# Optimization experiments

Hardware: AMD Instinct MI355X
Metric: run time of the kernel (lower is better)

## Reference

```python
import jax, jax.numpy as jnp
import numpy as np

EMBED_DIM = 1024
NUM_HEADS = 16
HEAD_DIM = EMBED_DIM // NUM_HEADS
RANK = 512
B, S = 4, 4096


def setup_inputs() -> dict:
    key = jax.random.key(0)
    ks = jax.random.split(key, 16)
    sd = 0.02
    inp = {
        "query": jax.random.normal(ks[0], (B, S, EMBED_DIM), jnp.float32),
        "key": jax.random.normal(ks[1], (B, S, EMBED_DIM), jnp.float32),
        "value": jax.random.normal(ks[2], (B, S, EMBED_DIM), jnp.float32),
        # torch nn.Linear weights: [out_features, in_features]
        "q_down_w": jax.random.normal(ks[3], (RANK, EMBED_DIM), jnp.float32) * sd,
        "q_up_w": jax.random.normal(ks[4], (EMBED_DIM, RANK), jnp.float32) * sd,
        "q_up_b": jax.random.normal(ks[5], (EMBED_DIM,), jnp.float32) * sd,
        "k_down_w": jax.random.normal(ks[6], (RANK, EMBED_DIM), jnp.float32) * sd,
        "k_up_w": jax.random.normal(ks[7], (EMBED_DIM, RANK), jnp.float32) * sd,
        "k_up_b": jax.random.normal(ks[8], (EMBED_DIM,), jnp.float32) * sd,
        "v_down_w": jax.random.normal(ks[9], (RANK, EMBED_DIM), jnp.float32) * sd,
        "v_up_w": jax.random.normal(ks[10], (EMBED_DIM, RANK), jnp.float32) * sd,
        "v_up_b": jax.random.normal(ks[11], (EMBED_DIM,), jnp.float32) * sd,
        "out_w": jax.random.normal(ks[12], (EMBED_DIM, EMBED_DIM), jnp.float32) * sd,
        "out_b": jax.random.normal(ks[13], (EMBED_DIM,), jnp.float32) * sd,
    }
    return inp


def _linear(x, w, b=None):
    y = x @ w.T
    return y if b is None else y + b


def reference(query, key, value,
              q_down_w, q_up_w, q_up_b,
              k_down_w, k_up_w, k_up_b,
              v_down_w, v_up_w, v_up_b,
              out_w, out_b):
    b, s, _ = query.shape
    # low-rank QKV projections
    q = _linear(_linear(query, q_down_w), q_up_w, q_up_b)
    k = _linear(_linear(key, k_down_w), k_up_w, k_up_b)
    v = _linear(_linear(value, v_down_w), v_up_w, v_up_b)
    # [B,S,E] -> [B,H,S,Dh]
    q = q.reshape(b, s, NUM_HEADS, HEAD_DIM).transpose(0, 2, 1, 3)
    k = k.reshape(b, s, NUM_HEADS, HEAD_DIM).transpose(0, 2, 1, 3)
    v = v.reshape(b, s, NUM_HEADS, HEAD_DIM).transpose(0, 2, 1, 3)
    # kernel feature map: elu + 1  (note: scaling_factor in original is computed but unused)
    q = jax.nn.elu(q) + 1.0
    k = jax.nn.elu(k) + 1.0
    k_sum = k.sum(axis=-2)                              # [B,H,Dh]
    denom = jnp.einsum('bhnd,bhd->bhn', q, k_sum)       # [B,H,S]
    kv = jnp.einsum('bhnd,bhne->bhde', k, v)            # [B,H,Dh,Dh]
    num = jnp.einsum('bhnd,bhde->bhne', q, kv)          # [B,H,S,Dh]
    out = num / (denom[..., None] + 1e-6)
    out = out.transpose(0, 2, 1, 3).reshape(b, s, EMBED_DIM)
    return _linear(out, out_w, out_b)
```

## Files before the change

### kernel.cpp

```cpp
#include <hip/hip_runtime.h>
#include <hip/hip_bf16.h>

typedef unsigned short ushort_t;
typedef unsigned int uint_t;
typedef __attribute__((ext_vector_type(8))) short short8;
typedef __attribute__((ext_vector_type(4))) float f32x4;
typedef __attribute__((ext_vector_type(2))) float f32x2;

#define EMBED 1024
#define RANK  512
#define BB    4
#define SS    4096
#define HH    16
#define DHD   64
#define MM    (BB*SS)
#define NCHUNK 16

__device__ __forceinline__ float bf2f(ushort_t u) {
    union { uint_t i; float f; } v; v.i = ((uint_t)u) << 16; return v.f;
}
__device__ __forceinline__ float asf(uint_t u) {
    union { uint_t i; float f; } v; v.i = u; return v.f;
}
__device__ __forceinline__ ushort_t f2bf(float f) {
    union { float f; uint_t i; } v; v.f = f;
    uint_t r = v.i + 0x7FFFu + ((v.i >> 16) & 1u);
    return (ushort_t)(r >> 16);
}
__device__ __forceinline__ uint_t cvtpk(float lo, float hi) {
    uint_t r;
    asm("v_cvt_pk_bf16_f32 %0, %1, %2" : "=v"(r) : "v"(lo), "v"(hi));
    return r;
}
__device__ __forceinline__ void gl2lds16(const void* g, void* l) {
    __builtin_amdgcn_global_load_lds((const __attribute__((address_space(1))) void*)g,
                                     (__attribute__((address_space(3))) void*)l,
                                     16, 0, 0);
}

template<int EPI>
__global__ __launch_bounds__(256) void gemm_bt(
    const ushort_t* __restrict__ A0, const ushort_t* __restrict__ A1, const ushort_t* __restrict__ A2,
    const ushort_t* __restrict__ B0, const ushort_t* __restrict__ B1, const ushort_t* __restrict__ B2,
    const float* __restrict__ bias0, const float* __restrict__ bias1, const float* __restrict__ bias2,
    void* __restrict__ C0, void* __restrict__ C1, void* __restrict__ C2,
    int N, int K, int nbx)
{
    __shared__ __align__(16) char lds_raw[49152];

    const int z = blockIdx.z;
    const ushort_t* Ab   = (z == 0) ? A0 : (z == 1) ? A1 : A2;
    const ushort_t* Bm   = (z == 0) ? B0 : (z == 1) ? B1 : B2;
    const float*    bias = (z == 0) ? bias0 : (z == 1) ? bias1 : bias2;
    void*           Cv   = (z == 0) ? C0 : (z == 1) ? C1 : C2;

    const int cpx = gridDim.x >> 3;
    const int bid = blockIdx.x;
    const int wg  = (bid & 7) * cpx + (bid >> 3);
    const long m0 = (long)(wg / nbx) * 128;
    const long n0 = (long)(wg % nbx) * 128;

    const int t = threadIdx.x;
    const int lane = t & 63;
    const int w = t >> 6;
    const int wr = (w >> 1) * 64;
    const int wc = (w & 1) * 64;
    const int fr = lane & 15;
    const int kq = (lane >> 4) * 8;

    const int srow = t >> 2;
    const int scol = ((t & 3) ^ ((srow >> 1) & 3)) * 8;
    const int kqs = (((kq >> 3) ^ ((fr >> 1) & 3))) * 8;

    auto STAGE = [&](int k0, int buf) {
        char* Ad = lds_raw + buf * 8192;
        char* Bd = lds_raw + 24576 + buf * 8192;
        #pragma unroll
        for (int ro = 0; ro < 2; ++ro) {
            const int row = ro * 64 + srow;
            gl2lds16(Ab + (m0 + row) * (long)K + k0 + scol, Ad + (ro * 256 + w * 64) * 16);
            gl2lds16(Bm + (n0 + row) * (long)K + k0 + scol, Bd + (ro * 256 + w * 64) * 16);
        }
    };

    f32x4 acc[4][4] = {};
    const int nt = K >> 5;

    STAGE(0, 0);
    STAGE(32, 1);

    int cur = 0;
    for (int ti = 0; ti < nt; ++ti) {
        if (ti + 1 < nt) { asm volatile("s_waitcnt vmcnt(4)" ::: "memory"); }
        else             { asm volatile("s_waitcnt vmcnt(0)" ::: "memory"); }
        __builtin_amdgcn_sched_barrier(0);
        __builtin_amdgcn_s_barrier();
        __builtin_amdgcn_sched_barrier(0);

        int nb = cur + 2; if (nb >= 3) nb -= 3;
        if (ti + 2 < nt) STAGE((ti + 2) << 5, nb);

        const ushort_t* Asc = (const ushort_t*)(lds_raw + cur * 8192);
        const ushort_t* Bsc = (const ushort_t*)(lds_raw + 24576 + cur * 8192);
        short8 av[4], bv[4];
        #pragma unroll
        for (int mi = 0; mi < 4; ++mi)
            av[mi] = *(const short8*)&Asc[(wr + mi * 16 + fr) * 32 + kqs];
        #pragma unroll
        for (int nf = 0; nf < 4; ++nf)
            bv[nf] = *(const short8*)&Bsc[(wc + nf * 16 + fr) * 32 + kqs];
        #pragma unroll
        for (int mi = 0; mi < 4; ++mi)
            #pragma unroll
            for (int nf = 0; nf < 4; ++nf)
                acc[mi][nf] = __builtin_amdgcn_mfma_f32_16x16x32_bf16(
                    av[mi], bv[nf], acc[mi][nf], 0, 0, 0);

        ++cur; if (cur == 3) cur = 0;
    }

    const int rj = (lane >> 4) * 4;
    if (EPI == 3) {
        float* Cf = (float*)Cv;
        __syncthreads();
        #pragma unroll
        for (int nf = 0; nf < 4; ++nf) {
            const long col = n0 + wc + nf * 16 + fr;
            const float bval = bias[col];
            #pragma unroll
            for (int mi = 0; mi < 4; ++mi)
                #pragma unroll
                for (int j = 0; j < 4; ++j)
                    Cf[(m0 + wr + mi * 16 + rj + j) * (long)N + col] = acc[mi][nf][j] + bval;
        }
    } else {
        ushort_t* Ct = (ushort_t*)lds_raw;
        __syncthreads();
        const bool do_elu = (EPI == 2) && (z < 2);
        #pragma unroll
        for (int nf = 0; nf < 4; ++nf) {
            const int coll = wc + nf * 16 + fr;
            const float bval = (EPI >= 2) ? bias[n0 + coll] : 0.0f;
            #pragma unroll
            for (int mi = 0; mi < 4; ++mi) {
                #pragma unroll
                for (int j = 0; j < 4; ++j) {
                    float x = acc[mi][nf][j];
                    if (EPI >= 2) x += bval;
                    if (do_elu) x = (x > 0.0f) ? (x + 1.0f) : __expf(x);
                    Ct[(wr + mi * 16 + rj + j) * 136 + coll] = f2bf(x);
                }
            }
        }
        __syncthreads();
        ushort_t* Cb = (ushort_t*)Cv;
        #pragma unroll
        for (int it = 0; it < 8; ++it) {
            const int idx = it * 256 + t;
            const int r   = idx >> 4;
            const int c8  = (idx & 15) * 8;
            short8 vv = *(const short8*)&Ct[r * 136 + c8];
            *(short8*)(Cb + (m0 + r) * (long)N + n0 + c8) = vv;
        }
    }
}

__global__ __launch_bounds__(256) void gemm_dn(
    const float* __restrict__ A0, const float* __restrict__ A1, const float* __restrict__ A2,
    const ushort_t* __restrict__ B0, const ushort_t* __restrict__ B1, const ushort_t* __restrict__ B2,
    void* __restrict__ C0, void* __restrict__ C1, void* __restrict__ C2,
    int N, int K, int nbx)
{
    __shared__ __align__(16) char lds_raw[73728];

    const int z = blockIdx.z;
    const float*    Af = (z == 0) ? A0 : (z == 1) ? A1 : A2;
    const ushort_t* Bm = (z == 0) ? B0 : (z == 1) ? B1 : B2;
    void*           Cv = (z == 0) ? C0 : (z == 1) ? C1 : C2;

    const int cpx = gridDim.x >> 3;
    const int bid = blockIdx.x;
    const int wg  = (bid & 7) * cpx + (bid >> 3);
    const long m0 = (long)(wg / nbx) * 128;
    const long n0 = (long)(wg % nbx) * 128;

    const int t = threadIdx.x;
    const int lane = t & 63;
    const int w = t >> 6;
    const int wr = (w >> 1) * 64;
    const int wc = (w & 1) * 64;
    const int fr = lane & 15;
    const int kq4 = lane >> 4;
    const int fx  = fr & 7;

    const int srow = t >> 2;
    const int scol = ((t & 3) ^ ((srow >> 1) & 3)) * 8;
    const int kqs = ((kq4 ^ ((fr >> 1) & 3))) * 8;

    const int sArow = t >> 3;
    const int sAcol = ((t & 7) ^ (sArow & 7)) * 4;

    auto STAGE = [&](int k0, int buf) {
        char* Ad = lds_raw + buf * 16384;
        char* Bd = lds_raw + 49152 + buf * 8192;
        #pragma unroll
        for (int p = 0; p < 4; ++p)
            gl2lds16(Af + (m0 + p * 32 + sArow) * (long)K + k0 + sAcol,
                     Ad + p * 4096 + w * 1024);
        #pragma unroll
        for (int ro = 0; ro < 2; ++ro)
            gl2lds16(Bm + (n0 + ro * 64 + srow) * (long)K + k0 + scol,
                     Bd + (ro * 256 + w * 64) * 16);
    };

    f32x4 acc[4][4] = {};
    const int nt = K >> 5;

    STAGE(0, 0);
    STAGE(32, 1);

    int cur = 0;
    for (int ti = 0; ti < nt; ++ti) {
        if (ti + 1 < nt) { asm volatile("s_waitcnt vmcnt(6)" ::: "memory"); }
        else             { asm volatile("s_waitcnt vmcnt(0)" ::: "memory"); }
        __builtin_amdgcn_sched_barrier(0);
        __builtin_amdgcn_s_barrier();
        __builtin_amdgcn_sched_barrier(0);

        int nb = cur + 2; if (nb >= 3) nb -= 3;
        if (ti + 2 < nt) STAGE((ti + 2) << 5, nb);

        const float*    Asf = (const float*)(lds_raw + cur * 16384);
        const ushort_t* Bsc = (const ushort_t*)(lds_raw + 49152 + cur * 8192);

        short8 av[4], bv[4];
        #pragma unroll
        for (int mi = 0; mi < 4; ++mi) {
            const int rowoff = (wr + mi * 16 + fr) * 32;
            const int s0 = (2 * kq4) ^ fx;
            const int s1 = (2 * kq4 + 1) ^ fx;
            f32x4 a0 = *(const f32x4*)&Asf[rowoff + s0 * 4];
            f32x4 a1 = *(const f32x4*)&Asf[rowoff + s1 * 4];
            union { uint_t u[4]; short8 s; } pk;
            pk.u[0] = cvtpk(a0[0], a0[1]);
            pk.u[1] = cvtpk(a0[2], a0[3]);
            pk.u[2] = cvtpk(a1[0], a1[1]);
            pk.u[3] = cvtpk(a1[2], a1[3]);
            av[mi] = pk.s;
        }
        #pragma unroll
        for (int nf = 0; nf < 4; ++nf)
            bv[nf] = *(const short8*)&Bsc[(wc + nf * 16 + fr) * 32 + kqs];
        #pragma unroll
        for (int mi = 0; mi < 4; ++mi)
            #pragma unroll
            for (int nf = 0; nf < 4; ++nf)
                acc[mi][nf] = __builtin_amdgcn_mfma_f32_16x16x32_bf16(
                    av[mi], bv[nf], acc[mi][nf], 0, 0, 0);

        ++cur; if (cur == 3) cur = 0;
    }

    const int rj = kq4 * 4;
    ushort_t* Ct = (ushort_t*)lds_raw;
    __syncthreads();
    #pragma unroll
    for (int nf = 0; nf < 4; ++nf) {
        const int coll = wc + nf * 16 + fr;
        #pragma unroll
        for (int mi = 0; mi < 4; ++mi)
            #pragma unroll
            for (int j = 0; j < 4; ++j)
                Ct[(wr + mi * 16 + rj + j) * 136 + coll] = f2bf(acc[mi][nf][j]);
    }
    __syncthreads();
    ushort_t* Cb = (ushort_t*)Cv;
    #pragma unroll
    for (int it = 0; it < 8; ++it) {
        const int idx = it * 256 + t;
        const int r   = idx >> 4;
        const int c8  = (idx & 15) * 8;
        short8 vv = *(const short8*)&Ct[r * 136 + c8];
        *(short8*)(Cb + (m0 + r) * (long)N + n0 + c8) = vv;
    }
}

__global__ __launch_bounds__(256) void cvt_weights(
    const float* __restrict__ s0, const float* __restrict__ s1,
    const float* __restrict__ s2, const float* __restrict__ s3,
    const float* __restrict__ s4, const float* __restrict__ s5,
    const float* __restrict__ s6,
    ushort_t* __restrict__ d0, ushort_t* __restrict__ d1,
    ushort_t* __restrict__ d2, ushort_t* __restrict__ d3,
    ushort_t* __restrict__ d4, ushort_t* __restrict__ d5,
    ushort_t* __restrict__ d6)
{
    const int y = blockIdx.y;
    const float* src; ushort_t* dst; int n;
    switch (y) {
        case 0: src = s0; dst = d0; n = RANK * EMBED; break;
        case 1: src = s1; dst = d1; n = RANK * EMBED; break;
        case 2: src = s2; dst = d2; n = RANK * EMBED; break;
        case 3: src = s3; dst = d3; n = RANK * EMBED; break;
        case 4: src = s4; dst = d4; n = RANK * EMBED; break;
        case 5: src = s5; dst = d5; n = RANK * EMBED; break;
        default: src = s6; dst = d6; n = EMBED * EMBED; break;
    }
    const int i = (blockIdx.x * 256 + threadIdx.x) * 4;
    if (i < n) {
        f32x4 f = *(const f32x4*)(src + i);
        typedef __attribute__((ext_vector_type(4))) short short4v;
        short4v h;
        h[0] = (short)f2bf(f[0]); h[1] = (short)f2bf(f[1]);
        h[2] = (short)f2bf(f[2]); h[3] = (short)f2bf(f[3]);
        *(short4v*)(dst + i) = h;
    }
}

__global__ __launch_bounds__(256) void kv_stats(const ushort_t* __restrict__ Kp,
                                                const ushort_t* __restrict__ Vp,
                                                float* __restrict__ kvp,
                                                float* __restrict__ ksump)
{
    __shared__ __align__(16) ushort_t Ks[64 * 64];
    __shared__ __align__(16) ushort_t Vs[64 * 64];
    const int t = threadIdx.x;
    const int w = t >> 6;
    const int bh = blockIdx.x;
    const int chunk = blockIdx.y;
    const int b = bh >> 4, h = bh & 15;
    const int d0 = (t & 15) * 4;
    const int e0 = (t >> 4) * 4;
    f32x2 acc2[4][2] = {};
    f32x2 sks2[2] = {};
    const long hbase = ((long)b * SS) * EMBED + h * DHD;

    for (int sub = 0; sub < 4; ++sub) {
        const int n00 = chunk * 256 + sub * 64;
        #pragma unroll
        for (int ro = 0; ro < 2; ++ro) {
            const int idx = ro * 256 + t;
            const int r = idx >> 3, c16 = idx & 7;
            const long g = hbase + (long)(n00 + r) * EMBED + c16 * 8;
            gl2lds16(Kp + g, (char*)Ks + (ro * 256 + w * 64) * 16);
            gl2lds16(Vp + g, (char*)Vs + (ro * 256 + w * 64) * 16);
        }
        __syncthreads();
        #pragma unroll 8
        for (int n = 0; n < 64; ++n) {
            const uint_t* kr = (const uint_t*)(Ks + n * 64 + d0);
            const uint_t* vr = (const uint_t*)(Vs + n * 64 + e0);
            const uint_t k01 = kr[0], k23 = kr[1];
            const uint_t v01 = vr[0], v23 = vr[1];
            f32x2 kd0, kd1;
            kd0[0] = asf(k01 << 16); kd0[1] = asf(k01 & 0xffff0000u);
            kd1[0] = asf(k23 << 16); kd1[1] = asf(k23 & 0xffff0000u);
            float ve[4];
            ve[0] = asf(v01 << 16); ve[1] = asf(v01 & 0xffff0000u);
            ve[2] = asf(v23 << 16); ve[3] = asf(v23 & 0xffff0000u);
            #pragma unroll
            for (int e = 0; e < 4; ++e) {
                f32x2 vb; vb[0] = ve[e]; vb[1] = ve[e];
                acc2[e][0] += vb * kd0;
                acc2[e][1] += vb * kd1;
            }
            if (e0 == 0) { sks2[0] += kd0; sks2[1] += kd1; }
        }
        __syncthreads();
    }

    float* dst = kvp + ((long)chunk * 64 + bh) * 4096;
    #pragma unroll
    for (int e = 0; e < 4; ++e) {
        f32x4 vv;
        vv[0] = acc2[e][0][0]; vv[1] = acc2[e][0][1];
        vv[2] = acc2[e][1][0]; vv[3] = acc2[e][1][1];
        *(f32x4*)(dst + (e0 + e) * 64 + d0) = vv;
    }
    if (e0 == 0) {
        float* sd = ksump + ((long)chunk * 64 + bh) * 64 + d0;
        sd[0] = sks2[0][0]; sd[1] = sks2[0][1];
        sd[2] = sks2[1][0]; sd[3] = sks2[1][1];
    }
}

__global__ __launch_bounds__(256) void kv_reduce(const float* __restrict__ kvp,
                                                 const float* __restrict__ ksump,
                                                 ushort_t* __restrict__ kvb,
                                                 float* __restrict__ ksumf)
{
    const int bh = blockIdx.x;
    const int t = threadIdx.x;
    const long base = (long)bh * 4096 + t * 16;
    f32x4 s[4] = {};
    #pragma unroll 4
    for (int c = 0; c < NCHUNK; ++c) {
        const float* src = kvp + (long)c * 64 * 4096 + base;
        #pragma unroll
        for (int j = 0; j < 4; ++j) s[j] += *(const f32x4*)(src + j * 4);
    }
    short8 o0, o1;
    #pragma unroll
    for (int j = 0; j < 4; ++j) {
        o0[j]     = (short)f2bf(s[0][j]); o0[4 + j] = (short)f2bf(s[1][j]);
        o1[j]     = (short)f2bf(s[2][j]); o1[4 + j] = (short)f2bf(s[3][j]);
    }
    *(short8*)(kvb + base)     = o0;
    *(short8*)(kvb + base + 8) = o1;

    if (t < 64) {
        float ss = 0.f;
        #pragma unroll
        for (int c = 0; c < NCHUNK; ++c) ss += ksump[(long)c * 64 * 64 + bh * 64 + t];
        ksumf[bh * 64 + t] = ss;
    }
}

__global__ __launch_bounds__(256) void attn_out(const ushort_t* __restrict__ Qp,
                                                const ushort_t* __restrict__ kvb,
                                                const float* __restrict__ ksum,
                                                ushort_t* __restrict__ Op)
{
    __shared__ __align__(16) ushort_t Qs[128 * 64];
    __shared__ __align__(16) ushort_t KVs[64 * 64];
    __shared__ float kss[64];
    __shared__ float dnm[128];
    const int t = threadIdx.x;
    const int w = t >> 6, lane = t & 63;
    const int bh = blockIdx.x, mc = blockIdx.y;
    const int b = bh >> 4, h = bh & 15;
    const long base = ((long)b * SS + mc * 128) * EMBED + h * DHD;

    #pragma unroll
    for (int ro = 0; ro < 4; ++ro) {
        const int idx = ro * 256 + t;
        const int r = idx >> 3, c16 = idx & 7;
        gl2lds16(Qp + base + (long)r * EMBED + c16 * 8,
                 (char*)Qs + (ro * 256 + w * 64) * 16);
    }
    #pragma unroll
    for (int ro = 0; ro < 2; ++ro) {
        const int idx = ro * 256 + t;
        gl2lds16(kvb + (long)bh * 4096 + idx * 8,
                 (char*)KVs + (ro * 256 + w * 64) * 16);
    }
    if (t < 64) kss[t] = ksum[bh * 64 + t];
    __syncthreads();

    if (t < 128) {
        float s = 0.f;
        const uint_t* qr = (const uint_t*)(Qs + t * 64);
        #pragma unroll
        for (int jj = 0; jj < 32; ++jj) {
            const uint_t u = qr[jj];
            union { uint_t i; float f; } lo, hi;
            lo.i = u << 16; hi.i = u & 0xffff0000u;
            s += lo.f * kss[2 * jj] + hi.f * kss[2 * jj + 1];
        }
        dnm[t] = s;
    }

    const int fr = lane & 15, kq = (lane >> 4) * 8;
    f32x4 acc[2][4] = {};
    #pragma unroll
    for (int ks = 0; ks < 2; ++ks) {
        short8 av[2], bv[4];
        #pragma unroll
        for (int mi = 0; mi < 2; ++mi)
            av[mi] = *(const short8*)&Qs[(w * 32 + mi * 16 + fr) * 64 + ks * 32 + kq];
        #pragma unroll
        for (int nf = 0; nf < 4; ++nf)
            bv[nf] = *(const short8*)&KVs[(nf * 16 + fr) * 64 + ks * 32 + kq];
        #pragma unroll
        for (int mi = 0; mi < 2; ++mi)
            #pragma unroll
            for (int nf = 0; nf < 4; ++nf)
                acc[mi][nf] = __builtin_amdgcn_mfma_f32_16x16x32_bf16(
                    av[mi], bv[nf], acc[mi][nf], 0, 0, 0);
    }
    __syncthreads();

    const int rj = (lane >> 4) * 4;
    #pragma unroll
    for (int mi = 0; mi < 2; ++mi) {
        #pragma unroll
        for (int nf = 0; nf < 4; ++nf) {
            #pragma unroll
            for (int j = 0; j < 4; ++j) {
                const int r = w * 32 + mi * 16 + rj + j;
                const int c = nf * 16 + fr;
                const float x = acc[mi][nf][j] / (dnm[r] + 1e-6f);
                Op[base + (long)r * EMBED + c] = f2bf(x);
            }
        }
    }
}

extern "C" void kernel_launch(void* const* d_in, const int* in_sizes, int n_in,
                              void* d_out, int out_size, void* d_ws, size_t ws_size,
                              hipStream_t stream)
{
    (void)in_sizes; (void)n_in; (void)out_size; (void)ws_size;
    const float* query = (const float*)d_in[0];
    const float* key_  = (const float*)d_in[1];
    const float* value = (const float*)d_in[2];
    const float* q_dw  = (const float*)d_in[3];
    const float* q_uw  = (const float*)d_in[4];
    const float* q_ub  = (const float*)d_in[5];
    const float* k_dw  = (const float*)d_in[6];
    const float* k_uw  = (const float*)d_in[7];
    const float* k_ub  = (const float*)d_in[8];
    const float* v_dw  = (const float*)d_in[9];
    const float* v_uw  = (const float*)d_in[10];
    const float* v_ub  = (const float*)d_in[11];
    const float* o_w   = (const float*)d_in[12];
    const float* o_b   = (const float*)d_in[13];

    char* ws = (char*)d_ws;
    size_t off = 0;
    auto alloc = [&](size_t bytes) -> void* {
        void* p = ws + off;
        off += (bytes + 255) & ~(size_t)255;
        return p;
    };
    const size_t WSMALL = (size_t)RANK * EMBED;
    ushort_t* bw_qd = (ushort_t*)alloc(WSMALL * 2);
    ushort_t* bw_qu = (ushort_t*)alloc(WSMALL * 2);
    ushort_t* bw_kd = (ushort_t*)alloc(WSMALL * 2);
    ushort_t* bw_ku = (ushort_t*)alloc(WSMALL * 2);
    ushort_t* bw_vd = (ushort_t*)alloc(WSMALL * 2);
    ushort_t* bw_vu = (ushort_t*)alloc(WSMALL * 2);
    ushort_t* bw_o  = (ushort_t*)alloc((size_t)EMBED * EMBED * 2);
    ushort_t* PQ    = (ushort_t*)alloc((size_t)MM * EMBED * 2);
    ushort_t* PK    = (ushort_t*)alloc((size_t)MM * EMBED * 2);
    ushort_t* PV    = (ushort_t*)alloc((size_t)MM * EMBED * 2);
    ushort_t* Y1q   = (ushort_t*)alloc((size_t)MM * RANK * 2);
    ushort_t* Y1k   = (ushort_t*)alloc((size_t)MM * RANK * 2);
    ushort_t* Y1v   = (ushort_t*)alloc((size_t)MM * RANK * 2);
    float*    ksump = (float*)alloc((size_t)NCHUNK * 64 * 64 * 4);
    float*    ksumf = (float*)alloc((size_t)64 * 64 * 4);
    ushort_t* kvb   = (ushort_t*)alloc((size_t)64 * 64 * 64 * 2);

    float*    kvp = (float*)Y1q;
    ushort_t* O   = Y1k;

    const dim3 blk(256);

    cvt_weights<<<dim3(EMBED * EMBED / 1024, 7), blk, 0, stream>>>(
        q_dw, q_uw, k_dw, k_uw, v_dw, v_uw, o_w,
        bw_qd, bw_qu, bw_kd, bw_ku, bw_vd, bw_vu, bw_o);

    gemm_dn<<<dim3(MM / 128 * (RANK / 128), 1, 3), blk, 0, stream>>>(
        query, key_, value,
        bw_qd, bw_kd, bw_vd,
        Y1q, Y1k, Y1v,
        RANK, EMBED, RANK / 128);

    gemm_bt<2><<<dim3(MM / 128 * (EMBED / 128), 1, 3), blk, 0, stream>>>(
        Y1q, Y1k, Y1v,
        bw_qu, bw_ku, bw_vu,
        q_ub, k_ub, v_ub,
        PQ, PK, PV,
        EMBED, RANK, EMBED / 128);

    kv_stats<<<dim3(64, NCHUNK), blk, 0, stream>>>(PK, PV, kvp, ksump);
    kv_reduce<<<dim3(64), blk, 0, stream>>>(kvp, ksump, kvb, ksumf);
    attn_out<<<dim3(64, 32), blk, 0, stream>>>(PQ, kvb, ksumf, O);

    gemm_bt<3><<<dim3(MM / 128 * (EMBED / 128), 1, 1), blk, 0, stream>>>(
        O, nullptr, nullptr,
        bw_o, nullptr, nullptr,
        o_b, nullptr, nullptr,
        d_out, nullptr, nullptr,
        EMBED, EMBED, EMBED / 128);
}
```

Measured before the change: 302.3 us.

## Convert fp32 A tiles to bf16 in registers before LDS staging in gemm_dn

The down-projection GEMM used to copy fp32 A tiles straight into LDS and convert them to bf16 after each LDS read, once per wave fragment. It now loads A from global into registers, converts to bf16 once, and writes the packed bf16 into a triple-buffered LDS area. B keeps its direct global-to-LDS path. This halves A's LDS footprint and read traffic and drops the redundant per-fragment conversions, at the cost of more register pressure and manual vmcnt bookkeeping in a 2x-unrolled pipeline.

```diff
diff --git a/kernel.cpp b/kernel.cpp
--- a/kernel.cpp
+++ b/kernel.cpp
@@ -166,15 +166,15 @@
 }
 
 __global__ __launch_bounds__(256) void gemm_dn(
-    const float* __restrict__ A0, const float* __restrict__ A1, const float* __restrict__ A2,
+    const float* __restrict__ A0f, const float* __restrict__ A1f, const float* __restrict__ A2f,
     const ushort_t* __restrict__ B0, const ushort_t* __restrict__ B1, const ushort_t* __restrict__ B2,
     void* __restrict__ C0, void* __restrict__ C1, void* __restrict__ C2,
     int N, int K, int nbx)
 {
-    __shared__ __align__(16) char lds_raw[73728];
+    __shared__ __align__(16) char lds_raw[49152];
 
     const int z = blockIdx.z;
-    const float*    Af = (z == 0) ? A0 : (z == 1) ? A1 : A2;
+    const float*    Af = (z == 0) ? A0f : (z == 1) ? A1f : A2f;
     const ushort_t* Bm = (z == 0) ? B0 : (z == 1) ? B1 : B2;
     void*           Cv = (z == 0) ? C0 : (z == 1) ? C1 : C2;
 
@@ -190,64 +190,72 @@
     const int wr = (w >> 1) * 64;
     const int wc = (w & 1) * 64;
     const int fr = lane & 15;
-    const int kq4 = lane >> 4;
-    const int fx  = fr & 7;
+    const int kq = (lane >> 4) * 8;
 
     const int srow = t >> 2;
     const int scol = ((t & 3) ^ ((srow >> 1) & 3)) * 8;
-    const int kqs = ((kq4 ^ ((fr >> 1) & 3))) * 8;
-
-    const int sArow = t >> 3;
-    const int sAcol = ((t & 7) ^ (sArow & 7)) * 4;
-
-    auto STAGE = [&](int k0, int buf) {
-        char* Ad = lds_raw + buf * 16384;
-        char* Bd = lds_raw + 49152 + buf * 8192;
-        #pragma unroll
-        for (int p = 0; p < 4; ++p)
-            gl2lds16(Af + (m0 + p * 32 + sArow) * (long)K + k0 + sAcol,
-                     Ad + p * 4096 + w * 1024);
+    const int kqs = (((kq >> 3) ^ ((fr >> 1) & 3))) * 8;
+
+    const int arow = t >> 1;
+    const int ac   = t & 1;
+    const int asw  = (arow >> 1) & 3;
+    const int asl0 = (2 * ac) ^ asw;
+    const int asl1 = (2 * ac + 1) ^ asw;
+
+    auto LOADA = [&](int k0, f32x4 (&r)[4]) {
+        const float* src = Af + (m0 + arow) * (long)K + k0 + ac * 16;
+        r[0] = *(const f32x4*)(src);
+        r[1] = *(const f32x4*)(src + 4);
+        r[2] = *(const f32x4*)(src + 8);
+        r[3] = *(const f32x4*)(src + 12);
+    };
+    auto STAGE_B = [&](int k0, int buf) {
+        char* Bd = lds_raw + 24576 + buf * 8192;
         #pragma unroll
         for (int ro = 0; ro < 2; ++ro)
             gl2lds16(Bm + (n0 + ro * 64 + srow) * (long)K + k0 + scol,
                      Bd + (ro * 256 + w * 64) * 16);
     };
+    auto WRITEA = [&](const f32x4 (&r)[4], int buf) {
+        ushort_t* Ad = (ushort_t*)(lds_raw + buf * 8192);
+        union { uint_t u[4]; short8 s; } p0, p1;
+        p0.u[0] = cvtpk(r[0][0], r[0][1]); p0.u[1] = cvtpk(r[0][2], r[0][3]);
+        p0.u[2] = cvtpk(r[1][0], r[1][1]); p0.u[3] = cvtpk(r[1][2], r[1][3]);
+        p1.u[0] = cvtpk(r[2][0], r[2][1]); p1.u[1] = cvtpk(r[2][2], r[2][3]);
+        p1.u[2] = cvtpk(r[3][0], r[3][1]); p1.u[3] = cvtpk(r[3][2], r[3][3]);
+        *(short8*)&Ad[arow * 32 + asl0 * 8] = p0.s;
+        *(short8*)&Ad[arow * 32 + asl1 * 8] = p1.s;
+    };
 
     f32x4 acc[4][4] = {};
     const int nt = K >> 5;
 
-    STAGE(0, 0);
-    STAGE(32, 1);
-
-    int cur = 0;
-    for (int ti = 0; ti < nt; ++ti) {
-        if (ti + 1 < nt) { asm volatile("s_waitcnt vmcnt(6)" ::: "memory"); }
-        else             { asm volatile("s_waitcnt vmcnt(0)" ::: "memory"); }
+    f32x4 rA0[4], rA1[4];
+    LOADA(0,  rA0); WRITEA(rA0, 0);
+    LOADA(32, rA1); WRITEA(rA1, 1);
+    STAGE_B(0, 0);  STAGE_B(32, 1);
+    LOADA(64, rA0);
+    __syncthreads();
+
+    auto BODY = [&](int ti, f32x4 (&curR)[4], f32x4 (&nxtR)[4]) {
+        if (ti + 2 < nt)      { asm volatile("s_waitcnt vmcnt(6) lgkmcnt(0)" ::: "memory"); }
+        else if (ti + 1 < nt) { asm volatile("s_waitcnt vmcnt(2) lgkmcnt(0)" ::: "memory"); }
+        else                  { asm volatile("s_waitcnt vmcnt(0) lgkmcnt(0)" ::: "memory"); }
         __builtin_amdgcn_sched_barrier(0);
         __builtin_amdgcn_s_barrier();
         __builtin_amdgcn_sched_barrier(0);
 
-        int nb = cur + 2; if (nb >= 3) nb -= 3;
-        if (ti + 2 < nt) STAGE((ti + 2) << 5, nb);
-
-        const float*    Asf = (const float*)(lds_raw + cur * 16384);
-        const ushort_t* Bsc = (const ushort_t*)(lds_raw + 49152 + cur * 8192);
-
+        if (ti + 3 < nt) LOADA((ti + 3) << 5, nxtR);
+        int nb = ti + 2; nb -= (nb / 3) * 3;
+        if (ti + 2 < nt) STAGE_B((ti + 2) << 5, nb);
+
+        const int cs = ti - (ti / 3) * 3;
+        const ushort_t* Asc = (const ushort_t*)(lds_raw + cs * 8192);
+        const ushort_t* Bsc = (const ushort_t*)(lds_raw + 24576 + cs * 8192);
         short8 av[4], bv[4];
         #pragma unroll
-        for (int mi = 0; mi < 4; ++mi) {
-            const int rowoff = (wr + mi * 16 + fr) * 32;
-            const int s0 = (2 * kq4) ^ fx;
-            const int s1 = (2 * kq4 + 1) ^ fx;
-            f32x4 a0 = *(const f32x4*)&Asf[rowoff + s0 * 4];
-            f32x4 a1 = *(const f32x4*)&Asf[rowoff + s1 * 4];
-            union { uint_t u[4]; short8 s; } pk;
-            pk.u[0] = cvtpk(a0[0], a0[1]);
-            pk.u[1] = cvtpk(a0[2], a0[3]);
-            pk.u[2] = cvtpk(a1[0], a1[1]);
-            pk.u[3] = cvtpk(a1[2], a1[3]);
-            av[mi] = pk.s;
-        }
+        for (int mi = 0; mi < 4; ++mi)
+            av[mi] = *(const short8*)&Asc[(wr + mi * 16 + fr) * 32 + kqs];
         #pragma unroll
         for (int nf = 0; nf < 4; ++nf)
             bv[nf] = *(const short8*)&Bsc[(wc + nf * 16 + fr) * 32 + kqs];
@@ -258,10 +266,16 @@
                 acc[mi][nf] = __builtin_amdgcn_mfma_f32_16x16x32_bf16(
                     av[mi], bv[nf], acc[mi][nf], 0, 0, 0);
 
-        ++cur; if (cur == 3) cur = 0;
-    }
-
-    const int rj = kq4 * 4;
+        __builtin_amdgcn_sched_barrier(0);
+        if (ti + 2 < nt) WRITEA(curR, nb);
+    };
+
+    for (int ti = 0; ti < nt; ti += 2) {
+        BODY(ti,     rA0, rA1);
+        BODY(ti + 1, rA1, rA0);
+    }
+
+    const int rj = (lane >> 4) * 4;
     ushort_t* Ct = (ushort_t*)lds_raw;
     __syncthreads();
     #pragma unroll
```

Result: slower. 308.5 us (+2.1%).
